# Kernel tuning notes

Hardware: AMD Instinct MI355X
Metric: run time of the kernel (lower is better)

## Reference

```python
import jax, jax.numpy as jnp
import numpy as np

B, T, E, H = 64, 577, 768, 64
GRID_H, GRID_W = 24, 24
NUM_PREFIX = 1
N = GRID_H * GRID_W  # 576 patches
EPS = 1e-5


def setup_inputs() -> dict:
    key = jax.random.key(0)
    ks = jax.random.split(key, 12)
    s = lambda k, shape, fan: jax.random.normal(k, shape, jnp.float32) / np.sqrt(fan)
    return {
        "x": jax.random.normal(ks[0], (B, T, E), jnp.float32),
        "w_q": s(ks[1], (E, H), E),
        "w_k": s(ks[2], (E, H), E),
        "w_v": s(ks[3], (E, H), E),
        "q_gamma": jnp.ones((H,), jnp.float32),
        "q_beta": jnp.zeros((H,), jnp.float32),
        "k_gamma": jnp.ones((H,), jnp.float32),
        "k_beta": jnp.zeros((H,), jnp.float32),
        "w_sigma": s(ks[4], (H, 2), H),
        "b_sigma": jnp.zeros((2,), jnp.float32),
        "w_alpha": s(ks[5], (H, 1), H),
        "b_alpha": jnp.zeros((1,), jnp.float32),
    }


def _layernorm(x, gamma, beta):
    mu = jnp.mean(x, axis=-1, keepdims=True)
    var = jnp.mean(jnp.square(x - mu), axis=-1, keepdims=True)
    return (x - mu) * jax.lax.rsqrt(var + EPS) * gamma + beta


def _grid_sq_dists():
    # coords[i] = (row, col) of patch i; squared coordinate differences [N, N]
    coords = jnp.stack(
        jnp.meshgrid(jnp.arange(GRID_H), jnp.arange(GRID_W), indexing="ij"), axis=-1
    ).reshape(N, 2).astype(jnp.float32)
    diff = coords[:, None, :] - coords[None, :, :]  # [N, N, 2]
    dy2 = jnp.square(diff[..., 0])  # row diff squared
    dx2 = jnp.square(diff[..., 1])  # col diff squared
    return dx2, dy2


def reference(x, w_q, w_k, w_v, q_gamma, q_beta, k_gamma, k_beta,
              w_sigma, b_sigma, w_alpha, b_alpha):
    q = _layernorm(x @ w_q, q_gamma, q_beta)  # [B, T, H]
    k = _layernorm(x @ w_k, k_gamma, k_beta)  # [B, T, H]
    v = x @ w_v                               # [B, T, H]

    sim = jnp.einsum("bqh,bkh->bqk", q, k)    # [B, T, T]

    q_nc = q[:, NUM_PREFIX:, :]               # [B, N, H]
    alpha = jax.nn.softplus(q_nc @ w_alpha + b_alpha)[..., 0]  # [B, N]
    sigma = jax.nn.sigmoid(q_nc @ w_sigma + b_sigma)           # [B, N, 2]
    sx = sigma[..., 0]  # [B, N]
    sy = sigma[..., 1]

    dx2, dy2 = _grid_sq_dists()  # [N, N] each
    # Gaussian decay bias: query-patch p controls sigma; [B, N, N]
    G = jnp.exp(
        -dx2[None] / (2.0 * jnp.square(sx)[:, :, None])
        - dy2[None] / (2.0 * jnp.square(sy)[:, :, None])
    )
    S = alpha[:, :, None] * G

    sim = sim.at[:, NUM_PREFIX:, NUM_PREFIX:].add(S)

    scale = jnp.sqrt(jnp.float32(H))
    attn = jax.nn.softmax(sim / scale, axis=-1)
    return attn @ v  # [B, T, H]
```

## Files before the change

### kernel.cpp

```cpp
#include <hip/hip_runtime.h>
#include <math.h>

#define B_ 64
#define T_ 577
#define E_ 768
#define H_ 64
#define N_ 576
#define GW_ 24

typedef float f32x4 __attribute__((ext_vector_type(4)));
typedef __bf16 bf16x8 __attribute__((ext_vector_type(8)));
typedef __bf16 bf16x4 __attribute__((ext_vector_type(4)));

__device__ inline void split_bf16(float f, __bf16& h, __bf16& l) {
  h = (__bf16)f;
  l = (__bf16)(f - (float)h);
}

__global__ __launch_bounds__(256) void prep_w_kernel(
    const float* __restrict__ wq, const float* __restrict__ wk, const float* __restrict__ wv,
    __bf16* __restrict__ wsw_hi, __bf16* __restrict__ wsw_lo)
{
  int idx = blockIdx.x * 256 + threadIdx.x;
  int kk = idx & 31;
  int n  = (idx >> 5) % 192;
  int kc = idx / (192 * 32);
  int k  = kc * 32 + kk;
  const float* src = (n < 64) ? wq : ((n < 128) ? wk : wv);
  int nn = n & 63;
  float f = src[(size_t)k * 64 + nn];
  __bf16 h, l;
  split_bf16(f, h, l);
  wsw_hi[idx] = h;
  wsw_lo[idx] = l;
}

__global__ __launch_bounds__(256) void qkv_ln_kernel(
    const float* __restrict__ x,
    const __bf16* __restrict__ wsw_hi, const __bf16* __restrict__ wsw_lo,
    const float* __restrict__ qg, const float* __restrict__ qb,
    const float* __restrict__ kg, const float* __restrict__ kb,
    const float* __restrict__ wsig, const float* __restrict__ bsig,
    const float* __restrict__ walp, const float* __restrict__ balp,
    float* __restrict__ qo, float* __restrict__ ko, float* __restrict__ vo,
    float* __restrict__ alo, float* __restrict__ sxo, float* __restrict__ syo)
{
  __shared__ __align__(16) float smem[64*193 + 256];
  __bf16 (*A_hi)[32] = (__bf16 (*)[32])smem;
  __bf16 (*A_lo)[32] = (__bf16 (*)[32])(smem + 1024);
  __bf16 (*B_hi)[32] = (__bf16 (*)[32])(smem + 2048);
  __bf16 (*B_lo)[32] = (__bf16 (*)[32])(smem + 2048 + 3072);
  float (*Cs)[193]   = (float (*)[193])smem;
  float* mu_q = smem + 64*193;
  float* rs_q = mu_q + 64;
  float* mu_k = rs_q + 64;
  float* rs_k = mu_k + 64;

  const int tid  = threadIdx.x;
  const int lane = tid & 63;
  const int w    = tid >> 6;
  const int rowbase = blockIdx.x << 6;

  f32x4 acc[4][3];
  #pragma unroll
  for (int mt = 0; mt < 4; ++mt)
    #pragma unroll
    for (int nt = 0; nt < 3; ++nt)
      acc[mt][nt] = (f32x4){0.f, 0.f, 0.f, 0.f};

  const int m     = lane & 15;
  const int kfrag = (lane >> 4) * 8;

  #pragma unroll 1
  for (int kc = 0; kc < 24; ++kc) {
    __syncthreads();
    #pragma unroll
    for (int i = 0; i < 2; ++i) {
      int s = tid + 256*i;
      int row = s >> 3, k4 = (s & 7) * 4;
      float4 xv = *(const float4*)(x + (size_t)(rowbase + row)*E_ + kc*32 + k4);
      __bf16 h0,l0,h1,l1,h2,l2,h3,l3;
      split_bf16(xv.x, h0, l0); split_bf16(xv.y, h1, l1);
      split_bf16(xv.z, h2, l2); split_bf16(xv.w, h3, l3);
      *(bf16x4*)&A_hi[row][k4] = (bf16x4){h0,h1,h2,h3};
      *(bf16x4*)&A_lo[row][k4] = (bf16x4){l0,l1,l2,l3};
    }
    #pragma unroll
    for (int i = 0; i < 3; ++i) {
      int e = tid + 256*i;
      bf16x8 hv = *(const bf16x8*)(wsw_hi + (size_t)kc*6144 + e*8);
      bf16x8 lv = *(const bf16x8*)(wsw_lo + (size_t)kc*6144 + e*8);
      *(bf16x8*)(((__bf16*)B_hi) + e*8) = hv;
      *(bf16x8*)(((__bf16*)B_lo) + e*8) = lv;
    }
    __syncthreads();

    bf16x8 bh[3], bl[3];
    #pragma unroll
    for (int nt = 0; nt < 3; ++nt) {
      int n = w*48 + nt*16 + m;
      bh[nt] = *(const bf16x8*)&B_hi[n][kfrag];
      bl[nt] = *(const bf16x8*)&B_lo[n][kfrag];
    }
    #pragma unroll
    for (int mt = 0; mt < 4; ++mt) {
      bf16x8 ah = *(const bf16x8*)&A_hi[mt*16 + m][kfrag];
      bf16x8 al = *(const bf16x8*)&A_lo[mt*16 + m][kfrag];
      #pragma unroll
      for (int nt = 0; nt < 3; ++nt) {
        acc[mt][nt] = __builtin_amdgcn_mfma_f32_16x16x32_bf16(ah, bh[nt], acc[mt][nt], 0, 0, 0);
        acc[mt][nt] = __builtin_amdgcn_mfma_f32_16x16x32_bf16(al, bh[nt], acc[mt][nt], 0, 0, 0);
        acc[mt][nt] = __builtin_amdgcn_mfma_f32_16x16x32_bf16(ah, bl[nt], acc[mt][nt], 0, 0, 0);
      }
    }
  }
  __syncthreads();

  #pragma unroll
  for (int mt = 0; mt < 4; ++mt)
    #pragma unroll
    for (int nt = 0; nt < 3; ++nt) {
      int row = mt*16 + (lane >> 4)*4;
      int col = w*48 + nt*16 + (lane & 15);
      Cs[row + 0][col] = acc[mt][nt].x;
      Cs[row + 1][col] = acc[mt][nt].y;
      Cs[row + 2][col] = acc[mt][nt].z;
      Cs[row + 3][col] = acc[mt][nt].w;
    }
  __syncthreads();

  if (tid < 64) {
    float s = 0.f;
    for (int h = 0; h < 64; ++h) s += Cs[tid][h];
    float mu = s * (1.f/64.f);
    float vs = 0.f;
    for (int h = 0; h < 64; ++h) { float d = Cs[tid][h] - mu; vs += d*d; }
    float rs = rsqrtf(vs*(1.f/64.f) + 1e-5f);
    mu_q[tid] = mu; rs_q[tid] = rs;

    s = 0.f;
    for (int h = 0; h < 64; ++h) s += Cs[tid][64+h];
    float mu2 = s * (1.f/64.f);
    vs = 0.f;
    for (int h = 0; h < 64; ++h) { float d = Cs[tid][64+h] - mu2; vs += d*d; }
    float rs2 = rsqrtf(vs*(1.f/64.f) + 1e-5f);
    mu_k[tid] = mu2; rs_k[tid] = rs2;

    int mrow = rowbase + tid;
    int tindex = mrow % T_;
    if (tindex >= 1) {
      int bb = mrow / T_;
      int g = tindex - 1;
      float za = 0.f, z0 = 0.f, z1 = 0.f;
      for (int h = 0; h < 64; ++h) {
        float qv = (Cs[tid][h] - mu) * rs * qg[h] + qb[h];
        za += qv * walp[h];
        z0 += qv * wsig[2*h];
        z1 += qv * wsig[2*h+1];
      }
      za += balp[0]; z0 += bsig[0]; z1 += bsig[1];
      float al = fmaxf(za, 0.f) + log1pf(__expf(-fabsf(za)));
      float sx = 1.f/(1.f + __expf(-z0));
      float sy = 1.f/(1.f + __expf(-z1));
      alo[bb*N_ + g] = al;
      sxo[bb*N_ + g] = 0.5f/(sx*sx);
      syo[bb*N_ + g] = 0.5f/(sy*sy);
    }
  }
  __syncthreads();
  for (int idx = tid; idx < 64*192; idx += 256) {
    int r = idx / 192, c = idx - (idx/192)*192;
    float val = Cs[r][c];
    size_t row = (size_t)rowbase + r;
    if (c < 64) {
      qo[row*64 + c] = (val - mu_q[r]) * rs_q[r] * qg[c] + qb[c];
    } else if (c < 128) {
      int h = c - 64;
      ko[row*64 + h] = (val - mu_k[r]) * rs_k[r] * kg[h] + kb[h];
    } else {
      vo[row*64 + (c-128)] = val;
    }
  }
}

__global__ __launch_bounds__(256) void attn_kernel(
    const float* __restrict__ q, const float* __restrict__ k, const float* __restrict__ v,
    const float* __restrict__ ala, const float* __restrict__ sxa, const float* __restrict__ sya,
    float* __restrict__ out)
{
  __shared__ __align__(16) __bf16 sm[8*4608];
  __shared__ float prm_al[64], prm_sx[64], prm_sy[64], prm_gr[64], prm_gc[64];
  __shared__ int   prm_has[64];

  __bf16* QH = sm;            __bf16* QL = sm + 4608;
  __bf16* KH = sm + 2*4608;   __bf16* KL = sm + 3*4608;
  __bf16* VH = sm + 4*4608;   __bf16* VL = sm + 5*4608;
  __bf16* PH = sm + 6*4608;   __bf16* PL = sm + 7*4608;

  const int tid  = threadIdx.x;
  const int lane = tid & 63;
  const int w    = tid >> 6;
  const int quad = lane >> 4;
  const int mrow = lane & 15;
  const int b    = blockIdx.y;
  const int qt   = blockIdx.x;

  const float* qbase = q + (size_t)b * T_ * H_;
  const float* kbase = k + (size_t)b * T_ * H_;
  const float* vbase = v + (size_t)b * T_ * H_;

  if (tid < 64) {
    int row = qt*64 + tid;
    float al=0.f, isx=0.f, isy=0.f, gr=0.f, gc=0.f; int has = 0;
    if (row >= 1 && row < T_) {
      int g = row - 1;
      al  = ala[b*N_ + g] * 0.125f;
      isx = sxa[b*N_ + g];
      isy = sya[b*N_ + g];
      gr  = (float)(g / GW_);
      gc  = (float)(g - (g/GW_)*GW_);
      has = 1;
    }
    prm_al[tid]=al; prm_sx[tid]=isx; prm_sy[tid]=isy;
    prm_gr[tid]=gr; prm_gc[tid]=gc; prm_has[tid]=has;
  }
  #pragma unroll
  for (int i = 0; i < 4; ++i) {
    int s = tid + 256*i;
    int r = s >> 4, c4 = (s & 15)*4;
    int row = qt*64 + r;
    int rowc = row < T_ ? row : T_ - 1;
    float4 v4 = *(const float4*)(qbase + (size_t)rowc*H_ + c4);
    v4.x *= 0.125f; v4.y *= 0.125f; v4.z *= 0.125f; v4.w *= 0.125f;
    __bf16 h0,l0,h1,l1,h2,l2,h3,l3;
    split_bf16(v4.x,h0,l0); split_bf16(v4.y,h1,l1);
    split_bf16(v4.z,h2,l2); split_bf16(v4.w,h3,l3);
    *(bf16x4*)&QH[r*72 + c4] = (bf16x4){h0,h1,h2,h3};
    *(bf16x4*)&QL[r*72 + c4] = (bf16x4){l0,l1,l2,l3};
  }
  __syncthreads();

  float p_al[4], p_sx[4], p_sy[4], p_gr[4], p_gc[4]; int p_has[4];
  #pragma unroll
  for (int reg = 0; reg < 4; ++reg) {
    int rr = w*16 + quad*4 + reg;
    p_al[reg]=prm_al[rr]; p_sx[reg]=prm_sx[rr]; p_sy[reg]=prm_sy[rr];
    p_gr[reg]=prm_gr[rr]; p_gc[reg]=prm_gc[rr]; p_has[reg]=prm_has[rr];
  }

  float mo[4], lsum[4], O_[4][4];
  #pragma unroll
  for (int reg = 0; reg < 4; ++reg) { mo[reg] = -INFINITY; lsum[reg] = 0.f; }
  #pragma unroll
  for (int nt = 0; nt < 4; ++nt)
    #pragma unroll
    for (int reg = 0; reg < 4; ++reg) O_[nt][reg] = 0.f;

  #pragma unroll 1
  for (int kt = 0; kt < 10; ++kt) {
    __syncthreads();
    #pragma unroll
    for (int i = 0; i < 4; ++i) {
      int s = tid + 256*i;
      int key = s >> 4, c4 = (s & 15)*4;
      int kgl = kt*64 + key;
      int kcl = kgl < T_ ? kgl : T_ - 1;
      float4 kv = *(const float4*)(kbase + (size_t)kcl*H_ + c4);
      __bf16 h0,l0,h1,l1,h2,l2,h3,l3;
      split_bf16(kv.x,h0,l0); split_bf16(kv.y,h1,l1);
      split_bf16(kv.z,h2,l2); split_bf16(kv.w,h3,l3);
      *(bf16x4*)&KH[key*72 + c4] = (bf16x4){h0,h1,h2,h3};
      *(bf16x4*)&KL[key*72 + c4] = (bf16x4){l0,l1,l2,l3};
    }
    {
      int d0 = tid & 15, k0 = (tid >> 4) * 4;
      #pragma unroll
      for (int di = 0; di < 3 + 1; ++di) {
        int dim = d0 + 16*di;
        float vv[4];
        #pragma unroll
        for (int ki = 0; ki < 4; ++ki) {
          int kgl = kt*64 + k0 + ki;
          int kcl = kgl < T_ ? kgl : T_ - 1;
          vv[ki] = vbase[(size_t)kcl*H_ + dim];
        }
        __bf16 h0,l0,h1,l1,h2,l2,h3,l3;
        split_bf16(vv[0],h0,l0); split_bf16(vv[1],h1,l1);
        split_bf16(vv[2],h2,l2); split_bf16(vv[3],h3,l3);
        *(bf16x4*)&VH[dim*72 + k0] = (bf16x4){h0,h1,h2,h3};
        *(bf16x4*)&VL[dim*72 + k0] = (bf16x4){l0,l1,l2,l3};
      }
    }
    __syncthreads();

    float S_[4][4];
    {
      f32x4 sac[4];
      #pragma unroll
      for (int nt = 0; nt < 4; ++nt) sac[nt] = (f32x4){0.f,0.f,0.f,0.f};
      #pragma unroll
      for (int ks = 0; ks < 2; ++ks) {
        int ko_ = ks*32 + quad*8;
        bf16x8 qh = *(const bf16x8*)&QH[(w*16 + mrow)*72 + ko_];
        bf16x8 ql = *(const bf16x8*)&QL[(w*16 + mrow)*72 + ko_];
        #pragma unroll
        for (int nt = 0; nt < 4; ++nt) {
          bf16x8 kh = *(const bf16x8*)&KH[(nt*16 + mrow)*72 + ko_];
          bf16x8 kl = *(const bf16x8*)&KL[(nt*16 + mrow)*72 + ko_];
          sac[nt] = __builtin_amdgcn_mfma_f32_16x16x32_bf16(qh, kh, sac[nt], 0, 0, 0);
          sac[nt] = __builtin_amdgcn_mfma_f32_16x16x32_bf16(ql, kh, sac[nt], 0, 0, 0);
          sac[nt] = __builtin_amdgcn_mfma_f32_16x16x32_bf16(qh, kl, sac[nt], 0, 0, 0);
        }
      }
      #pragma unroll
      for (int nt = 0; nt < 4; ++nt) {
        S_[nt][0] = sac[nt].x; S_[nt][1] = sac[nt].y;
        S_[nt][2] = sac[nt].z; S_[nt][3] = sac[nt].w;
      }
    }

    #pragma unroll
    for (int nt = 0; nt < 4; ++nt) {
      int keyg = kt*64 + nt*16 + mrow;
      bool kval = keyg < T_;
      bool khas = (keyg >= 1) && kval;
      float kgf = (float)(keyg - 1);
      float krf = floorf(kgf * (1.0f/24.0f));
      float kcf = kgf - 24.f*krf;
      #pragma unroll
      for (int reg = 0; reg < 4; ++reg) {
        float sval = S_[nt][reg];
        float dx = p_gc[reg] - kcf, dy = p_gr[reg] - krf;
        float bias = p_al[reg] * __expf(-(dx*dx*p_sx[reg] + dy*dy*p_sy[reg]));
        sval += (khas && p_has[reg]) ? bias : 0.f;
        S_[nt][reg] = kval ? sval : -1e30f;
      }
    }

    float mt_[4], lt_[4], sc_[4], mn_[4];
    #pragma unroll
    for (int reg = 0; reg < 4; ++reg) {
      float mx = fmaxf(fmaxf(S_[0][reg], S_[1][reg]), fmaxf(S_[2][reg], S_[3][reg]));
      mx = fmaxf(mx, __shfl_xor(mx, 1, 64));
      mx = fmaxf(mx, __shfl_xor(mx, 2, 64));
      mx = fmaxf(mx, __shfl_xor(mx, 4, 64));
      mx = fmaxf(mx, __shfl_xor(mx, 8, 64));
      mt_[reg] = mx;
      mn_[reg] = fmaxf(mo[reg], mx);
      lt_[reg] = 0.f;
    }
    #pragma unroll
    for (int nt = 0; nt < 4; ++nt)
      #pragma unroll
      for (int reg = 0; reg < 4; ++reg) {
        float p = __expf(S_[nt][reg] - mn_[reg]);
        S_[nt][reg] = p;
        lt_[reg] += p;
      }
    #pragma unroll
    for (int reg = 0; reg < 4; ++reg) {
      float ls = lt_[reg];
      ls += __shfl_xor(ls, 1, 64);
      ls += __shfl_xor(ls, 2, 64);
      ls += __shfl_xor(ls, 4, 64);
      ls += __shfl_xor(ls, 8, 64);
      sc_[reg] = __expf(mo[reg] - mn_[reg]);
      lsum[reg] = lsum[reg]*sc_[reg] + ls;
      mo[reg] = mn_[reg];
    }
    #pragma unroll
    for (int nt = 0; nt < 4; ++nt)
      #pragma unroll
      for (int reg = 0; reg < 4; ++reg) O_[nt][reg] *= sc_[reg];

    #pragma unroll
    for (int nt = 0; nt < 4; ++nt)
      #pragma unroll
      for (int reg = 0; reg < 4; ++reg) {
        float p = S_[nt][reg];
        __bf16 ph, pl;
        split_bf16(p, ph, pl);
        int addr = (w*16 + quad*4 + reg)*72 + nt*16 + mrow;
        PH[addr] = ph;
        PL[addr] = pl;
      }

    #pragma unroll
    for (int nt = 0; nt < 4; ++nt) {
      f32x4 c = (f32x4){O_[nt][0], O_[nt][1], O_[nt][2], O_[nt][3]};
      #pragma unroll
      for (int ks = 0; ks < 2; ++ks) {
        int ko_ = ks*32 + quad*8;
        bf16x8 pah = *(const bf16x8*)&PH[(w*16 + mrow)*72 + ko_];
        bf16x8 pall = *(const bf16x8*)&PL[(w*16 + mrow)*72 + ko_];
        bf16x8 vh = *(const bf16x8*)&VH[(nt*16 + mrow)*72 + ko_];
        bf16x8 vl = *(const bf16x8*)&VL[(nt*16 + mrow)*72 + ko_];
        c = __builtin_amdgcn_mfma_f32_16x16x32_bf16(pah, vh, c, 0, 0, 0);
        c = __builtin_amdgcn_mfma_f32_16x16x32_bf16(pall, vh, c, 0, 0, 0);
        c = __builtin_amdgcn_mfma_f32_16x16x32_bf16(pah, vl, c, 0, 0, 0);
      }
      O_[nt][0] = c.x; O_[nt][1] = c.y; O_[nt][2] = c.z; O_[nt][3] = c.w;
    }
  }

  #pragma unroll
  for (int reg = 0; reg < 4; ++reg) {
    int rowg = qt*64 + w*16 + quad*4 + reg;
    if (rowg < T_) {
      float inv = 1.f / lsum[reg];
      #pragma unroll
      for (int nt = 0; nt < 4; ++nt) {
        out[((size_t)b*T_ + rowg)*H_ + nt*16 + mrow] = O_[nt][reg] * inv;
      }
    }
  }
}

extern "C" void kernel_launch(void* const* d_in, const int* in_sizes, int n_in,
                              void* d_out, int out_size, void* d_ws, size_t ws_size,
                              hipStream_t stream) {
  const float* x      = (const float*)d_in[0];
  const float* wq     = (const float*)d_in[1];
  const float* wk     = (const float*)d_in[2];
  const float* wv     = (const float*)d_in[3];
  const float* qg     = (const float*)d_in[4];
  const float* qb     = (const float*)d_in[5];
  const float* kg     = (const float*)d_in[6];
  const float* kb     = (const float*)d_in[7];
  const float* wsig   = (const float*)d_in[8];
  const float* bsig   = (const float*)d_in[9];
  const float* walp   = (const float*)d_in[10];
  const float* balp   = (const float*)d_in[11];
  float* out = (float*)d_out;

  float* ws  = (float*)d_ws;
  const size_t nrow = (size_t)B_ * T_;
  float* qo  = ws;
  float* ko  = qo + nrow*H_;
  float* vo  = ko + nrow*H_;
  float* alo = vo + nrow*H_;
  float* sxo = alo + (size_t)B_*N_;
  float* syo = sxo + (size_t)B_*N_;
  __bf16* wsw_hi = (__bf16*)(syo + (size_t)B_*N_);
  __bf16* wsw_lo = wsw_hi + 24*192*32;

  hipLaunchKernelGGL(prep_w_kernel, dim3(576), dim3(256), 0, stream,
                     wq, wk, wv, wsw_hi, wsw_lo);
  hipLaunchKernelGGL(qkv_ln_kernel, dim3(577), dim3(256), 0, stream,
                     x, wsw_hi, wsw_lo, qg, qb, kg, kb, wsig, bsig, walp, balp,
                     qo, ko, vo, alo, sxo, syo);
  hipLaunchKernelGGL(attn_kernel, dim3(10, B_), dim3(256), 0, stream,
                     qo, ko, vo, alo, sxo, syo, out);
}
```

Baseline: 297.9 us.

## Prefetch next global tiles into registers and pad LDS rows in QKV and attention

Both the QKV projection GEMM and the attention loop now load the next K-chunk or K/V tile from global memory into registers while the current tile is computed, then split and store it to LDS after the barrier. This hides global load latency behind MFMA work. The QKV shared tiles are padded to a stride of 40 to reduce LDS bank conflicts. LayerNorm statistics for q and k are computed by separate thread groups, and the epilogue writes float4s. The weight prep kernel now has each thread handle 32 k-values with vectorised stores, at the cost of more registers per thread.

After: 289.4 us. -2.9%, faster.

```diff
diff --git a/kernel.cpp b/kernel.cpp
--- a/kernel.cpp
+++ b/kernel.cpp
@@ -21,18 +21,23 @@
     const float* __restrict__ wq, const float* __restrict__ wk, const float* __restrict__ wv,
     __bf16* __restrict__ wsw_hi, __bf16* __restrict__ wsw_lo)
 {
-  int idx = blockIdx.x * 256 + threadIdx.x;
-  int kk = idx & 31;
-  int n  = (idx >> 5) % 192;
-  int kc = idx / (192 * 32);
-  int k  = kc * 32 + kk;
+  int t = blockIdx.x * 256 + threadIdx.x;
+  if (t >= 24*192) return;
+  int kc = t / 192, n = t - (t/192)*192;
   const float* src = (n < 64) ? wq : ((n < 128) ? wk : wv);
   int nn = n & 63;
-  float f = src[(size_t)k * 64 + nn];
-  __bf16 h, l;
-  split_bf16(f, h, l);
-  wsw_hi[idx] = h;
-  wsw_lo[idx] = l;
+  __bf16 hbuf[32], lbuf[32];
+  #pragma unroll
+  for (int kk = 0; kk < 32; ++kk) {
+    float f = src[(size_t)(kc*32 + kk)*64 + nn];
+    split_bf16(f, hbuf[kk], lbuf[kk]);
+  }
+  size_t base = (size_t)t * 32;
+  #pragma unroll
+  for (int i = 0; i < 4; ++i) {
+    *(bf16x8*)(wsw_hi + base + i*8) = *(bf16x8*)&hbuf[i*8];
+    *(bf16x8*)(wsw_lo + base + i*8) = *(bf16x8*)&lbuf[i*8];
+  }
 }
 
 __global__ __launch_bounds__(256) void qkv_ln_kernel(
@@ -46,11 +51,11 @@
     float* __restrict__ alo, float* __restrict__ sxo, float* __restrict__ syo)
 {
   __shared__ __align__(16) float smem[64*193 + 256];
-  __bf16 (*A_hi)[32] = (__bf16 (*)[32])smem;
-  __bf16 (*A_lo)[32] = (__bf16 (*)[32])(smem + 1024);
-  __bf16 (*B_hi)[32] = (__bf16 (*)[32])(smem + 2048);
-  __bf16 (*B_lo)[32] = (__bf16 (*)[32])(smem + 2048 + 3072);
-  float (*Cs)[193]   = (float (*)[193])smem;
+  __bf16* A_hi = (__bf16*)smem;
+  __bf16* A_lo = A_hi + 64*40;
+  __bf16* B_hi = A_lo + 64*40;
+  __bf16* B_lo = B_hi + 192*40;
+  float (*Cs)[193] = (float (*)[193])smem;
   float* mu_q = smem + 64*193;
   float* rs_q = mu_q + 64;
   float* mu_k = rs_q + 64;
@@ -71,41 +76,60 @@
   const int m     = lane & 15;
   const int kfrag = (lane >> 4) * 8;
 
+  float4 xr0, xr1;
+  bf16x8 whr[3], wlr[3];
+  const int s0 = tid, s1 = tid + 256;
+  const int arow0 = s0 >> 3, ak0 = (s0 & 7) * 4;
+  const int arow1 = s1 >> 3, ak1 = (s1 & 7) * 4;
+
+  auto load_chunk = [&](int kc) {
+    xr0 = *(const float4*)(x + (size_t)(rowbase + arow0)*E_ + kc*32 + ak0);
+    xr1 = *(const float4*)(x + (size_t)(rowbase + arow1)*E_ + kc*32 + ak1);
+    #pragma unroll
+    for (int i = 0; i < 3; ++i) {
+      int e = tid + 256*i;
+      whr[i] = *(const bf16x8*)(wsw_hi + (size_t)kc*6144 + e*8);
+      wlr[i] = *(const bf16x8*)(wsw_lo + (size_t)kc*6144 + e*8);
+    }
+  };
+  auto store_chunk = [&]() {
+    __bf16 h0,l0,h1,l1,h2,l2,h3,l3;
+    split_bf16(xr0.x,h0,l0); split_bf16(xr0.y,h1,l1);
+    split_bf16(xr0.z,h2,l2); split_bf16(xr0.w,h3,l3);
+    *(bf16x4*)&A_hi[arow0*40 + ak0] = (bf16x4){h0,h1,h2,h3};
+    *(bf16x4*)&A_lo[arow0*40 + ak0] = (bf16x4){l0,l1,l2,l3};
+    split_bf16(xr1.x,h0,l0); split_bf16(xr1.y,h1,l1);
+    split_bf16(xr1.z,h2,l2); split_bf16(xr1.w,h3,l3);
+    *(bf16x4*)&A_hi[arow1*40 + ak1] = (bf16x4){h0,h1,h2,h3};
+    *(bf16x4*)&A_lo[arow1*40 + ak1] = (bf16x4){l0,l1,l2,l3};
+    #pragma unroll
+    for (int i = 0; i < 3; ++i) {
+      int e = tid + 256*i;
+      int n = e >> 2, g = e & 3;
+      *(bf16x8*)&B_hi[n*40 + g*8] = whr[i];
+      *(bf16x8*)&B_lo[n*40 + g*8] = wlr[i];
+    }
+  };
+
+  load_chunk(0);
   #pragma unroll 1
   for (int kc = 0; kc < 24; ++kc) {
     __syncthreads();
-    #pragma unroll
-    for (int i = 0; i < 2; ++i) {
-      int s = tid + 256*i;
-      int row = s >> 3, k4 = (s & 7) * 4;
-      float4 xv = *(const float4*)(x + (size_t)(rowbase + row)*E_ + kc*32 + k4);
-      __bf16 h0,l0,h1,l1,h2,l2,h3,l3;
-      split_bf16(xv.x, h0, l0); split_bf16(xv.y, h1, l1);
-      split_bf16(xv.z, h2, l2); split_bf16(xv.w, h3, l3);
-      *(bf16x4*)&A_hi[row][k4] = (bf16x4){h0,h1,h2,h3};
-      *(bf16x4*)&A_lo[row][k4] = (bf16x4){l0,l1,l2,l3};
-    }
-    #pragma unroll
-    for (int i = 0; i < 3; ++i) {
-      int e = tid + 256*i;
-      bf16x8 hv = *(const bf16x8*)(wsw_hi + (size_t)kc*6144 + e*8);
-      bf16x8 lv = *(const bf16x8*)(wsw_lo + (size_t)kc*6144 + e*8);
-      *(bf16x8*)(((__bf16*)B_hi) + e*8) = hv;
-      *(bf16x8*)(((__bf16*)B_lo) + e*8) = lv;
-    }
+    store_chunk();
     __syncthreads();
+    if (kc < 23) load_chunk(kc + 1);
 
     bf16x8 bh[3], bl[3];
     #pragma unroll
     for (int nt = 0; nt < 3; ++nt) {
       int n = w*48 + nt*16 + m;
-      bh[nt] = *(const bf16x8*)&B_hi[n][kfrag];
-      bl[nt] = *(const bf16x8*)&B_lo[n][kfrag];
+      bh[nt] = *(const bf16x8*)&B_hi[n*40 + kfrag];
+      bl[nt] = *(const bf16x8*)&B_lo[n*40 + kfrag];
     }
     #pragma unroll
     for (int mt = 0; mt < 4; ++mt) {
-      bf16x8 ah = *(const bf16x8*)&A_hi[mt*16 + m][kfrag];
-      bf16x8 al = *(const bf16x8*)&A_lo[mt*16 + m][kfrag];
+      bf16x8 ah = *(const bf16x8*)&A_hi[(mt*16 + m)*40 + kfrag];
+      bf16x8 al = *(const bf16x8*)&A_lo[(mt*16 + m)*40 + kfrag];
       #pragma unroll
       for (int nt = 0; nt < 3; ++nt) {
         acc[mt][nt] = __builtin_amdgcn_mfma_f32_16x16x32_bf16(ah, bh[nt], acc[mt][nt], 0, 0, 0);
@@ -135,25 +159,31 @@
     float mu = s * (1.f/64.f);
     float vs = 0.f;
     for (int h = 0; h < 64; ++h) { float d = Cs[tid][h] - mu; vs += d*d; }
-    float rs = rsqrtf(vs*(1.f/64.f) + 1e-5f);
-    mu_q[tid] = mu; rs_q[tid] = rs;
-
-    s = 0.f;
-    for (int h = 0; h < 64; ++h) s += Cs[tid][64+h];
-    float mu2 = s * (1.f/64.f);
-    vs = 0.f;
-    for (int h = 0; h < 64; ++h) { float d = Cs[tid][64+h] - mu2; vs += d*d; }
-    float rs2 = rsqrtf(vs*(1.f/64.f) + 1e-5f);
-    mu_k[tid] = mu2; rs_k[tid] = rs2;
-
-    int mrow = rowbase + tid;
+    mu_q[tid] = mu;
+    rs_q[tid] = rsqrtf(vs*(1.f/64.f) + 1e-5f);
+  } else if (tid < 128) {
+    int r = tid - 64;
+    float s = 0.f;
+    for (int h = 0; h < 64; ++h) s += Cs[r][64+h];
+    float mu = s * (1.f/64.f);
+    float vs = 0.f;
+    for (int h = 0; h < 64; ++h) { float d = Cs[r][64+h] - mu; vs += d*d; }
+    mu_k[r] = mu;
+    rs_k[r] = rsqrtf(vs*(1.f/64.f) + 1e-5f);
+  }
+  __syncthreads();
+
+  if (tid >= 192) {
+    int r = tid - 192;
+    int mrow = rowbase + r;
     int tindex = mrow % T_;
     if (tindex >= 1) {
       int bb = mrow / T_;
       int g = tindex - 1;
+      float mu = mu_q[r], rs = rs_q[r];
       float za = 0.f, z0 = 0.f, z1 = 0.f;
       for (int h = 0; h < 64; ++h) {
-        float qv = (Cs[tid][h] - mu) * rs * qg[h] + qb[h];
+        float qv = (Cs[r][h] - mu) * rs * qg[h] + qb[h];
         za += qv * walp[h];
         z0 += qv * wsig[2*h];
         z1 += qv * wsig[2*h+1];
@@ -167,18 +197,29 @@
       syo[bb*N_ + g] = 0.5f/(sy*sy);
     }
   }
-  __syncthreads();
-  for (int idx = tid; idx < 64*192; idx += 256) {
-    int r = idx / 192, c = idx - (idx/192)*192;
-    float val = Cs[r][c];
+  for (int idx = tid; idx < 64*48; idx += 256) {
+    int r = idx / 48, c4 = (idx - (idx/48)*48) * 4;
     size_t row = (size_t)rowbase + r;
-    if (c < 64) {
-      qo[row*64 + c] = (val - mu_q[r]) * rs_q[r] * qg[c] + qb[c];
-    } else if (c < 128) {
-      int h = c - 64;
-      ko[row*64 + h] = (val - mu_k[r]) * rs_k[r] * kg[h] + kb[h];
+    float4 val = make_float4(Cs[r][c4], Cs[r][c4+1], Cs[r][c4+2], Cs[r][c4+3]);
+    if (c4 < 64) {
+      float mu = mu_q[r], rs = rs_q[r];
+      float4 o;
+      o.x = (val.x - mu)*rs*qg[c4+0] + qb[c4+0];
+      o.y = (val.y - mu)*rs*qg[c4+1] + qb[c4+1];
+      o.z = (val.z - mu)*rs*qg[c4+2] + qb[c4+2];
+      o.w = (val.w - mu)*rs*qg[c4+3] + qb[c4+3];
+      *(float4*)(qo + row*64 + c4) = o;
+    } else if (c4 < 128) {
+      int h = c4 - 64;
+      float mu = mu_k[r], rs = rs_k[r];
+      float4 o;
+      o.x = (val.x - mu)*rs*kg[h+0] + kb[h+0];
+      o.y = (val.y - mu)*rs*kg[h+1] + kb[h+1];
+      o.z = (val.z - mu)*rs*kg[h+2] + kb[h+2];
+      o.w = (val.w - mu)*rs*kg[h+3] + kb[h+3];
+      *(float4*)(ko + row*64 + h) = o;
     } else {
-      vo[row*64 + (c-128)] = val;
+      *(float4*)(vo + row*64 + (c4-128)) = val;
     }
   }
 }
@@ -256,42 +297,57 @@
     #pragma unroll
     for (int reg = 0; reg < 4; ++reg) O_[nt][reg] = 0.f;
 
-  #pragma unroll 1
-  for (int kt = 0; kt < 10; ++kt) {
-    __syncthreads();
+  float4 kreg[4];
+  float  vreg[16];
+  const int d0 = tid & 15, k0 = (tid >> 4) * 4;
+
+  auto load_kv = [&](int kt) {
     #pragma unroll
     for (int i = 0; i < 4; ++i) {
       int s = tid + 256*i;
       int key = s >> 4, c4 = (s & 15)*4;
       int kgl = kt*64 + key;
       int kcl = kgl < T_ ? kgl : T_ - 1;
-      float4 kv = *(const float4*)(kbase + (size_t)kcl*H_ + c4);
+      kreg[i] = *(const float4*)(kbase + (size_t)kcl*H_ + c4);
+    }
+    #pragma unroll
+    for (int di = 0; di < 4; ++di)
+      #pragma unroll
+      for (int ki = 0; ki < 4; ++ki) {
+        int kgl = kt*64 + k0 + ki;
+        int kcl = kgl < T_ ? kgl : T_ - 1;
+        vreg[di*4+ki] = vbase[(size_t)kcl*H_ + d0 + 16*di];
+      }
+  };
+  auto store_kv = [&]() {
+    #pragma unroll
+    for (int i = 0; i < 4; ++i) {
+      int s = tid + 256*i;
+      int key = s >> 4, c4 = (s & 15)*4;
       __bf16 h0,l0,h1,l1,h2,l2,h3,l3;
-      split_bf16(kv.x,h0,l0); split_bf16(kv.y,h1,l1);
-      split_bf16(kv.z,h2,l2); split_bf16(kv.w,h3,l3);
+      split_bf16(kreg[i].x,h0,l0); split_bf16(kreg[i].y,h1,l1);
+      split_bf16(kreg[i].z,h2,l2); split_bf16(kreg[i].w,h3,l3);
       *(bf16x4*)&KH[key*72 + c4] = (bf16x4){h0,h1,h2,h3};
       *(bf16x4*)&KL[key*72 + c4] = (bf16x4){l0,l1,l2,l3};
     }
-    {
-      int d0 = tid & 15, k0 = (tid >> 4) * 4;
-      #pragma unroll
-      for (int di = 0; di < 3 + 1; ++di) {
-        int dim = d0 + 16*di;
-        float vv[4];
-        #pragma unroll
-        for (int ki = 0; ki < 4; ++ki) {
-          int kgl = kt*64 + k0 + ki;
-          int kcl = kgl < T_ ? kgl : T_ - 1;
-          vv[ki] = vbase[(size_t)kcl*H_ + dim];
-        }
-        __bf16 h0,l0,h1,l1,h2,l2,h3,l3;
-        split_bf16(vv[0],h0,l0); split_bf16(vv[1],h1,l1);
-        split_bf16(vv[2],h2,l2); split_bf16(vv[3],h3,l3);
-        *(bf16x4*)&VH[dim*72 + k0] = (bf16x4){h0,h1,h2,h3};
-        *(bf16x4*)&VL[dim*72 + k0] = (bf16x4){l0,l1,l2,l3};
-      }
-    }
+    #pragma unroll
+    for (int di = 0; di < 4; ++di) {
+      int dim = d0 + 16*di;
+      __bf16 h0,l0,h1,l1,h2,l2,h3,l3;
+      split_bf16(vreg[di*4+0],h0,l0); split_bf16(vreg[di*4+1],h1,l1);
+      split_bf16(vreg[di*4+2],h2,l2); split_bf16(vreg[di*4+3],h3,l3);
+      *(bf16x4*)&VH[dim*72 + k0] = (bf16x4){h0,h1,h2,h3};
+      *(bf16x4*)&VL[dim*72 + k0] = (bf16x4){l0,l1,l2,l3};
+    }
+  };
+
+  load_kv(0);
+  #pragma unroll 1
+  for (int kt = 0; kt < 10; ++kt) {
     __syncthreads();
+    store_kv();
+    __syncthreads();
+    if (kt < 9) load_kv(kt + 1);
 
     float S_[4][4];
     {
@@ -337,7 +393,7 @@
       }
     }
 
-    float mt_[4], lt_[4], sc_[4], mn_[4];
+    float lt_[4], sc_[4], mn_[4];
     #pragma unroll
     for (int reg = 0; reg < 4; ++reg) {
       float mx = fmaxf(fmaxf(S_[0][reg], S_[1][reg]), fmaxf(S_[2][reg], S_[3][reg]));
@@ -345,7 +401,6 @@
       mx = fmaxf(mx, __shfl_xor(mx, 2, 64));
       mx = fmaxf(mx, __shfl_xor(mx, 4, 64));
       mx = fmaxf(mx, __shfl_xor(mx, 8, 64));
-      mt_[reg] = mx;
       mn_[reg] = fmaxf(mo[reg], mx);
       lt_[reg] = 0.f;
     }
@@ -391,10 +446,10 @@
       #pragma unroll
       for (int ks = 0; ks < 2; ++ks) {
         int ko_ = ks*32 + quad*8;
-        bf16x8 pah = *(const bf16x8*)&PH[(w*16 + mrow)*72 + ko_];
+        bf16x8 pah  = *(const bf16x8*)&PH[(w*16 + mrow)*72 + ko_];
         bf16x8 pall = *(const bf16x8*)&PL[(w*16 + mrow)*72 + ko_];
-        bf16x8 vh = *(const bf16x8*)&VH[(nt*16 + mrow)*72 + ko_];
-        bf16x8 vl = *(const bf16x8*)&VL[(nt*16 + mrow)*72 + ko_];
+        bf16x8 vh   = *(const bf16x8*)&VH[(nt*16 + mrow)*72 + ko_];
+        bf16x8 vl   = *(const bf16x8*)&VL[(nt*16 + mrow)*72 + ko_];
         c = __builtin_amdgcn_mfma_f32_16x16x32_bf16(pah, vh, c, 0, 0, 0);
         c = __builtin_amdgcn_mfma_f32_16x16x32_bf16(pall, vh, c, 0, 0, 0);
         c = __builtin_amdgcn_mfma_f32_16x16x32_bf16(pah, vl, c, 0, 0, 0);
@@ -444,7 +499,7 @@
   __bf16* wsw_hi = (__bf16*)(syo + (size_t)B_*N_);
   __bf16* wsw_lo = wsw_hi + 24*192*32;
 
-  hipLaunchKernelGGL(prep_w_kernel, dim3(576), dim3(256), 0, stream,
+  hipLaunchKernelGGL(prep_w_kernel, dim3(18), dim3(256), 0, stream,
                      wq, wk, wv, wsw_hi, wsw_lo);
   hipLaunchKernelGGL(qkv_ln_kernel, dim3(577), dim3(256), 0, stream,
                      x, wsw_hi, wsw_lo, qg, qb, kg, kb, wsig, bsig, walp, balp,
```
